# Kernel tuning notes

Hardware: AMD Instinct MI355X
Metric: run time of the kernel (lower is better)

Reference implementation:

```python
import jax, jax.numpy as jnp
import numpy as np

ALPHA = 0.2  # leaky_relu negative slope
NEG_INF = -9e15


def _gat_stage(x, adj_mask, W, a):
    """Multi-head dense GAT layer (concat=True).
    x: [N, Fin], adj_mask: [N, N] bool, W: [H, Fin, O], a: [H, 2*O].
    Returns [N, H*O].
    """
    O = W.shape[-1]
    Wh = jnp.einsum('nf,hfo->hno', x, W)                 # [H, N, O]
    f1 = jnp.einsum('hno,ho->hn', Wh, a[:, :O])          # a_src . Wh_i
    f2 = jnp.einsum('hno,ho->hn', Wh, a[:, O:])          # a_dst . Wh_j
    e = f1[:, :, None] + f2[:, None, :]                  # [H, N, N]
    e = jnp.where(e > 0, e, ALPHA * e)                   # leaky_relu
    e = jnp.where(adj_mask[None], e, NEG_INF)            # mask non-edges
    att = jax.nn.softmax(e, axis=-1)                     # row softmax over neighbors
    h = jnp.einsum('hnm,hmo->hno', att, Wh)              # aggregate
    h = jax.nn.elu(h)                                    # concat=True -> elu
    H, N, _ = h.shape
    return jnp.transpose(h, (1, 0, 2)).reshape(N, H * O)  # head concat


def setup_inputs() -> dict:
    key = jax.random.key(0)
    ks = jax.random.split(key, 12)
    N, F0, NHID, H, NCLASS = 4096, 512, 64, 4, 40
    x = jax.random.normal(ks[0], (N, F0), jnp.float32)
    adj = jax.random.randint(ks[1], (N, N), 0, 2, jnp.int32)
    s = 0.05
    W1 = jax.random.normal(ks[2], (H, F0, NHID), jnp.float32) * s
    a1 = jax.random.normal(ks[3], (H, 2 * NHID), jnp.float32) * s
    W2 = jax.random.normal(ks[4], (4, H * NHID, 32), jnp.float32) * s
    a2 = jax.random.normal(ks[5], (4, 64), jnp.float32) * s
    W3 = jax.random.normal(ks[6], (4, 4 * 32, 16), jnp.float32) * s
    a3 = jax.random.normal(ks[7], (4, 32), jnp.float32) * s
    Wlin = jax.random.normal(ks[8], (4 * 16, NCLASS), jnp.float32) * s
    blin = jnp.zeros((NCLASS,), jnp.float32)
    return {"x": x, "adj": adj, "W1": W1, "a1": a1, "W2": W2, "a2": a2,
            "W3": W3, "a3": a3, "Wlin": Wlin, "blin": blin}


def reference(x, adj, W1, a1, W2, a2, W3, a3, Wlin, blin):
    # eval mode: all F.dropout calls are identity
    m = adj > 0
    h = _gat_stage(x, m, W1, a1)    # [N, 256]
    h = _gat_stage(h, m, W2, a2)    # [N, 128]
    h = _gat_stage(h, m, W3, a3)    # [N, 64]
    logits = h @ Wlin + blin        # [N, nclass]
    return jax.nn.log_softmax(logits, axis=1)
```

## Files before the change

### kernel.cpp

```cpp
#include <hip/hip_runtime.h>
#include <hip/hip_bf16.h>
#include <stdint.h>

typedef __attribute__((ext_vector_type(8))) short short8;
typedef __attribute__((ext_vector_type(4))) float float4v;

#define NHEADS 4
#define NNODES 4096
#define LOG2E 1.4426950408889634f
#define NJS 8
#define PSTR ((size_t)NHEADS * NNODES * 64)
#define LSTR ((size_t)NHEADS * NNODES)

__device__ __forceinline__ unsigned short f2b(float x) {
    union { float f; uint32_t u; } v; v.f = x;
    uint32_t u = v.u;
    uint32_t r = (u + 0x7FFFu + ((u >> 16) & 1u)) >> 16;
    return (unsigned short)r;
}
__device__ __forceinline__ float b2f(unsigned short s) {
    union { uint32_t u; float f; } v; v.u = ((uint32_t)s) << 16;
    return v.f;
}
__device__ __forceinline__ uint32_t cvtpk(float lo, float hi) {
    uint32_t r;
    asm("v_cvt_pk_bf16_f32 %0, %1, %2" : "=v"(r) : "v"(lo), "v"(hi));
    return r;
}

#define AS1 __attribute__((address_space(1)))
#define AS3 __attribute__((address_space(3)))
__device__ __forceinline__ void gl_lds16(const void* g, void* l) {
    __builtin_amdgcn_global_load_lds((const AS1 unsigned int*)g,
                                     (AS3 unsigned int*)l, 16, 0, 0);
}

__global__ __launch_bounds__(256) void k_pre(const int* __restrict__ adj,
                                             unsigned short* __restrict__ mask16,
                                             const float* __restrict__ x,
                                             unsigned short* __restrict__ xbf,
                                             const float* __restrict__ W1,
                                             unsigned short* __restrict__ WT1,
                                             const float* __restrict__ W2,
                                             unsigned short* __restrict__ WT2,
                                             const float* __restrict__ W3,
                                             unsigned short* __restrict__ WT3) {
    int b = blockIdx.x;
    if (b < 4096) {
        const int4* ap = (const int4*)(adj + ((size_t)b << 12)) + threadIdx.x * 4;
        int4 a0 = ap[0], a1 = ap[1], a2 = ap[2], a3 = ap[3];
        int v[16] = {a0.x, a0.y, a0.z, a0.w, a1.x, a1.y, a1.z, a1.w,
                     a2.x, a2.y, a2.z, a2.w, a3.x, a3.y, a3.z, a3.w};
        uint32_t bits = 0;
#pragma unroll
        for (int k = 0; k < 16; ++k) bits |= (uint32_t)(v[k] != 0) << k;
        mask16[(b << 8) + threadIdx.x] = (unsigned short)bits;
        return;
    }
    int i = (b - 4096) * 256 + threadIdx.x;
    if (i < 524288) {
        float4v v = ((const float4v*)x)[i];
        uint2 r;
        r.x = cvtpk(v[0], v[1]);
        r.y = cvtpk(v[2], v[3]);
        ((uint2*)xbf)[i] = r;
    } else if (i < 524288 + 131072) {
        int j = i - 524288;
        int o = j & 63, f = (j >> 6) & 511, h = j >> 15;
        WT1[((size_t)(h * 64 + o)) * 512 + f] = f2b(W1[j]);
    } else if (i < 524288 + 131072 + 32768) {
        int j = i - 655360;
        int o = j & 31, f = (j >> 5) & 255, h = j >> 13;
        WT2[((size_t)(h * 32 + o)) * 256 + f] = f2b(W2[j]);
    } else if (i < 524288 + 131072 + 32768 + 8192) {
        int j = i - 688128;
        int o = j & 15, f = (j >> 4) & 127, h = j >> 11;
        WT3[((size_t)(h * 16 + o)) * 128 + f] = f2b(W3[j]);
    }
}

template <int Fin, int O>
__global__ __launch_bounds__(256) void k_whgemm(const unsigned short* __restrict__ A,
                                                const unsigned short* __restrict__ WT,
                                                const float* __restrict__ avec,
                                                unsigned short* __restrict__ WhT,
                                                float* __restrict__ f1,
                                                float* __restrict__ f2) {
    __shared__ float scc[4][16][64];
    constexpr int HPB = 64 / O;
    const int rt = blockIdx.x & 255, cg = blockIdx.x >> 8;
    const int wv = threadIdx.x >> 6, lane = threadIdx.x & 63;
    const int il = lane & 15, g = lane >> 4;
    constexpr int kpw = Fin >> 2;
    const int k0 = wv * kpw;
    float4v acc[4];
#pragma unroll
    for (int ot = 0; ot < 4; ++ot) acc[ot] = (float4v){0.f, 0.f, 0.f, 0.f};
    const unsigned short* Arow = A + (size_t)(rt * 16 + il) * Fin + k0 + 8 * g;
    const unsigned short* Bcol = WT + (size_t)(cg * 64 + il) * Fin + k0 + 8 * g;
#pragma unroll
    for (int k = 0; k < kpw; k += 32) {
        short8 af = *(const short8*)(Arow + k);
#pragma unroll
        for (int ot = 0; ot < 4; ++ot) {
            short8 bf = *(const short8*)(Bcol + (size_t)ot * 16 * Fin + k);
            acc[ot] = __builtin_amdgcn_mfma_f32_16x16x32_bf16(af, bf, acc[ot], 0, 0, 0);
        }
    }
#pragma unroll
    for (int ot = 0; ot < 4; ++ot)
#pragma unroll
        for (int r = 0; r < 4; ++r) scc[wv][g * 4 + r][ot * 16 + il] = acc[ot][r];
    __syncthreads();
    for (int e = threadIdx.x; e < 1024; e += 256) {
        int row = e >> 6, col = e & 63;
        float v = scc[0][row][col] + scc[1][row][col] + scc[2][row][col] + scc[3][row][col];
        int gc = cg * 64 + col;
        int hh = gc / O, o = gc % O;
        WhT[((size_t)(hh * O + o)) * NNODES + rt * 16 + row] = f2b(v);
    }
    {
        int hl = lane / O, o = lane % O;
        int h = cg * HPB + hl;
        float av1 = avec[h * 2 * O + o];
        float av2 = avec[h * 2 * O + O + o];
#pragma unroll
        for (int r = 0; r < 4; ++r) {
            int row = wv * 4 + r;
            float v = scc[0][row][lane] + scc[1][row][lane] + scc[2][row][lane] + scc[3][row][lane];
            float s1 = v * av1, s2 = v * av2;
#pragma unroll
            for (int d = O / 2; d > 0; d >>= 1) {
                s1 += __shfl_xor(s1, d);
                s2 += __shfl_xor(s2, d);
            }
            if (o == 0) {
                int n = rt * 16 + row;
                f1[h * NNODES + n] = s1 * LOG2E;
                f2[h * NNODES + n] = s2 * LOG2E;
            }
        }
    }
}

template <int O>
__global__ __launch_bounds__(256, 5)
void k_pv(const uint32_t* __restrict__ mask,
          const float* __restrict__ f1L,
          const float* __restrict__ f2L,
          const unsigned short* __restrict__ WhT,
          float* __restrict__ pacc,
          float* __restrict__ lpart) {
    constexpr int TJ  = (O == 16) ? 128 : 64;
    constexpr int NTT = 512 / TJ;
    constexpr int NT  = O / 16;
    constexpr int CH  = O * TJ / 8;
    constexpr int SPT = CH / 256;
    constexpr int CPR = TJ / 8;
    constexpr int NSUB = TJ / 32;
    __shared__ unsigned short bt[3][CH * 8];
    __shared__ float sf2[512];
    const int b = blockIdx.x;
    const int js = b & 7, rt = (b >> 3) & 63, h = b >> 9;
    const int tid = threadIdx.x, wv = tid >> 6, lane = tid & 63;
    const int il = lane & 15, g = lane >> 4;
    const int j0b = js * 512;
    const float* f2h = f2L + h * NNODES;
    const unsigned short* WB0 = WhT + (size_t)h * O * NNODES;
    const int nrow = wv * 16 + il;

    const float f1i = f1L[h * NNODES + rt * 64 + nrow];
    const uint32_t* mrow = mask + (size_t)(rt * 64 + nrow) * 128 + js * 16;
    uint32_t mw[16];
    {
        uint4 a = *(const uint4*)(mrow);
        uint4 c = *(const uint4*)(mrow + 4);
        uint4 d = *(const uint4*)(mrow + 8);
        uint4 e = *(const uint4*)(mrow + 12);
        mw[0] = a.x;  mw[1] = a.y;  mw[2] = a.z;  mw[3] = a.w;
        mw[4] = c.x;  mw[5] = c.y;  mw[6] = c.z;  mw[7] = c.w;
        mw[8] = d.x;  mw[9] = d.y;  mw[10] = d.z; mw[11] = d.w;
        mw[12] = e.x; mw[13] = e.y; mw[14] = e.z; mw[15] = e.w;
    }
    asm volatile("s_waitcnt vmcnt(0)" ::: "memory");
    __builtin_amdgcn_sched_barrier(0);

    auto stage_tile = [&](int t, int buf) {
#pragma unroll
        for (int q = 0; q < SPT; ++q) {
            int s = q * 256 + tid;
            int o = s / CPR, c = s % CPR;
            int cs = c ^ (o & (CPR - 1));
            gl_lds16(WB0 + (size_t)o * NNODES + j0b + t * TJ + 8 * cs,
                     (char*)&bt[buf][0] + s * 16);
        }
    };
    if (tid < 128) gl_lds16(f2h + j0b + tid * 4, (char*)sf2 + tid * 16);
    stage_tile(0, 0);
    stage_tile(1, 1);
    asm volatile("s_waitcnt vmcnt(%0)" :: "i"(SPT) : "memory");
    __builtin_amdgcn_sched_barrier(0);
    __builtin_amdgcn_s_barrier();

    float4v acc[NT];
#pragma unroll
    for (int ot = 0; ot < NT; ++ot) acc[ot] = (float4v){0.f, 0.f, 0.f, 0.f};
    float4v accl = (float4v){0.f, 0.f, 0.f, 0.f};
    short8 bones;
#pragma unroll
    for (int q = 0; q < 8; ++q) bones[q] = (il == 0) ? (short)0x3F80 : (short)0;

    auto compute = [&](int t) {
        const char* btc = (const char*)&bt[t % 3][0];
        const float* fp0 = sf2 + t * TJ + 8 * g;
#pragma unroll
        for (int s = 0; s < NSUB; ++s) {
            short8 B[NT];
#pragma unroll
            for (int ot = 0; ot < NT; ++ot) {
                int o = ot * 16 + il;
                B[ot] = *(const short8*)(btc + o * (CPR * 16) +
                                         16 * (((s << 2) + g) ^ (o & (CPR - 1))));
            }
            const float* fp = fp0 + s * 32;
            float4v fa = *(const float4v*)fp;
            float4v fb = *(const float4v*)(fp + 4);
            uint32_t word = mw[t * NSUB + s];
            uint32_t bits = (word >> (8 * g)) & 0xFFu;
            float p[8];
#pragma unroll
            for (int bb = 0; bb < 8; ++bb) {
                float sv = f1i + ((bb < 4) ? fa[bb] : fb[bb - 4]);
                sv = fmaxf(sv, 0.2f * sv);
                float pv = __builtin_amdgcn_exp2f(sv);
                p[bb] = ((bits >> bb) & 1u) ? pv : 0.f;
            }
            union { short8 s8; uint32_t u[4]; } pu;
            pu.u[0] = cvtpk(p[0], p[1]);
            pu.u[1] = cvtpk(p[2], p[3]);
            pu.u[2] = cvtpk(p[4], p[5]);
            pu.u[3] = cvtpk(p[6], p[7]);
#pragma unroll
            for (int ot = 0; ot < NT; ++ot)
                acc[ot] = __builtin_amdgcn_mfma_f32_16x16x32_bf16(pu.s8, B[ot], acc[ot], 0, 0, 0);
            accl = __builtin_amdgcn_mfma_f32_16x16x32_bf16(pu.s8, bones, accl, 0, 0, 0);
        }
    };

#pragma unroll
    for (int t = 0; t < NTT - 2; ++t) {
        stage_tile(t + 2, (t + 2) % 3);
        compute(t);
        asm volatile("s_waitcnt vmcnt(%0)" :: "i"(SPT) : "memory");
        __builtin_amdgcn_sched_barrier(0);
        __builtin_amdgcn_s_barrier();
    }
    compute(NTT - 2);
    asm volatile("s_waitcnt vmcnt(0)" ::: "memory");
    __builtin_amdgcn_sched_barrier(0);
    __builtin_amdgcn_s_barrier();
    compute(NTT - 1);

    float* pj = pacc + js * PSTR + (size_t)h * NNODES * O;
#pragma unroll
    for (int ot = 0; ot < NT; ++ot)
#pragma unroll
        for (int r = 0; r < 4; ++r)
            pj[(size_t)(rt * 64 + wv * 16 + g * 4 + r) * O + ot * 16 + il] = acc[ot][r];
    if (il == 0) {
        float* lj = lpart + js * LSTR + h * NNODES;
#pragma unroll
        for (int r = 0; r < 4; ++r)
            lj[rt * 64 + wv * 16 + g * 4 + r] = accl[r];
    }
}

template <int O>
__global__ __launch_bounds__(256) void k_fin(const float* __restrict__ pacc,
                                             const float* __restrict__ lpart,
                                             unsigned short* __restrict__ hout) {
    constexpr int HO = NHEADS * O;
    int e = blockIdx.x * 256 + threadIdx.x;
    int o = e % O;
    int n = (e / O) & (NNODES - 1);
    int h = e / (O * NNODES);
    size_t idx = ((size_t)h * NNODES + n) * O + o;
    int li = h * NNODES + n;
    float s = 0.f, l = 0.f;
#pragma unroll
    for (int k = 0; k < NJS; ++k) {
        s += pacc[k * PSTR + idx];
        l += lpart[k * LSTR + li];
    }
    float v = s / l;
    v = (v > 0.f) ? v : (__expf(v) - 1.f);
    hout[(size_t)n * HO + h * O + o] = f2b(v);
}

__global__ __launch_bounds__(256) void k_fin3final(const float* __restrict__ pacc,
                                                   const float* __restrict__ lpart,
                                                   const float* __restrict__ Wlin,
                                                   const float* __restrict__ blin,
                                                   float* __restrict__ out) {
    __shared__ float sh3[4][64];
    const int tid = threadIdx.x;
    const int n0 = blockIdx.x * 4;
    {
        int r = tid >> 6, hh = (tid >> 4) & 3, o = tid & 15;
        int n = n0 + r;
        size_t idx = ((size_t)hh * NNODES + n) * 16 + o;
        int li = hh * NNODES + n;
        float s = 0.f, l = 0.f;
#pragma unroll
        for (int k = 0; k < NJS; ++k) {
            s += pacc[k * PSTR + idx];
            l += lpart[k * LSTR + li];
        }
        float v = s / l;
        v = (v > 0.f) ? v : (__expf(v) - 1.f);
        sh3[r][hh * 16 + o] = v;
    }
    __syncthreads();
    int rr = tid >> 6, lane = tid & 63;
    int n = n0 + rr;
    float logit = 0.f;
    if (lane < 40) {
        logit = blin[lane];
#pragma unroll
        for (int k = 0; k < 64; ++k) logit += sh3[rr][k] * Wlin[k * 40 + lane];
    }
    float mv = (lane < 40) ? logit : -3.0e38f;
    for (int d = 32; d > 0; d >>= 1) mv = fmaxf(mv, __shfl_xor(mv, d));
    float ex = (lane < 40) ? __expf(logit - mv) : 0.f;
    for (int d = 32; d > 0; d >>= 1) ex += __shfl_xor(ex, d);
    if (lane < 40) out[n * 40 + lane] = logit - mv - logf(ex);
}

template <int Fin, int O>
static void run_stage(hipStream_t stream, const uint32_t* mask, const unsigned short* xin,
                      const unsigned short* WT, const float* avec,
                      unsigned short* WhT, float* f1, float* f2,
                      float* pacc, float* lpart) {
    constexpr int CG = (NHEADS * O) / 64;
    k_whgemm<Fin, O><<<256 * CG, 256, 0, stream>>>(xin, WT, avec, WhT, f1, f2);
    k_pv<O><<<4 * 64 * NJS, 256, 0, stream>>>(mask, f1, f2, WhT, pacc, lpart);
}

extern "C" void kernel_launch(void* const* d_in, const int* in_sizes, int n_in,
                              void* d_out, int out_size, void* d_ws, size_t ws_size,
                              hipStream_t stream) {
    const float* x    = (const float*)d_in[0];
    const int*   adj  = (const int*)d_in[1];
    const float* W1   = (const float*)d_in[2];
    const float* a1   = (const float*)d_in[3];
    const float* W2   = (const float*)d_in[4];
    const float* a2   = (const float*)d_in[5];
    const float* W3   = (const float*)d_in[6];
    const float* a3   = (const float*)d_in[7];
    const float* Wlin = (const float*)d_in[8];
    const float* blin = (const float*)d_in[9];
    float* out = (float*)d_out;

    char* ws = (char*)d_ws;
    uint32_t*       mask = (uint32_t*)ws;
    unsigned short* xbf  = (unsigned short*)(ws + (2u << 20));
    unsigned short* WhT  = (unsigned short*)(ws + (6u << 20));
    unsigned short* WT1  = (unsigned short*)(ws + (8u << 20));
    unsigned short* WT2  = (unsigned short*)(ws + (8u << 20) + (256u << 10));
    unsigned short* WT3  = (unsigned short*)(ws + (8u << 20) + (320u << 10));
    float*          f1   = (float*)(ws + (8u << 20) + (384u << 10));
    float*          f2   = (float*)(ws + (8u << 20) + (448u << 10));
    float*          lpart= (float*)(ws + (8u << 20) + (512u << 10));
    float*          pacc = (float*)(ws + (9u << 20));

    k_pre<<<4096 + 2720, 256, 0, stream>>>(adj, (unsigned short*)mask, x, xbf,
                                           W1, WT1, W2, WT2, W3, WT3);

    run_stage<512, 64>(stream, mask, xbf, WT1, a1, WhT, f1, f2, pacc, lpart);
    k_fin<64><<<NHEADS * NNODES * 64 / 256, 256, 0, stream>>>(pacc, lpart, xbf);
    run_stage<256, 32>(stream, mask, xbf, WT2, a2, WhT, f1, f2, pacc, lpart);
    k_fin<32><<<NHEADS * NNODES * 32 / 256, 256, 0, stream>>>(pacc, lpart, xbf);
    run_stage<128, 16>(stream, mask, xbf, WT3, a3, WhT, f1, f2, pacc, lpart);
    k_fin3final<<<NNODES / 4, 256, 0, stream>>>(pacc, lpart, Wlin, blin, out);
}
```

Baseline: 148.1 us.

## Halve j-splits in attention kernel and stage mask bits through LDS

The attention-aggregation kernel now splits the neighbor dimension into 4 chunks of 1024 instead of 8 chunks of 512. Each block covers twice as many tiles, and there are half as many partial accumulators to reduce later. Mask words are loaded cooperatively into a padded shared-memory array instead of 16 registers per thread, which frees registers for the longer loop. Compute sections are wrapped in s_setprio to favor MFMA issue. The cost is fewer blocks, an occupancy hint lowered from 5 to 4, and extra LDS reads for the mask. The combine step may also need to match the new NJS value.

```diff
diff --git a/kernel.cpp b/kernel.cpp
--- a/kernel.cpp
+++ b/kernel.cpp
@@ -8,7 +8,7 @@
 #define NHEADS 4
 #define NNODES 4096
 #define LOG2E 1.4426950408889634f
-#define NJS 8
+#define NJS 4
 #define PSTR ((size_t)NHEADS * NNODES * 64)
 #define LSTR ((size_t)NHEADS * NNODES)
 
@@ -17,10 +17,6 @@
     uint32_t u = v.u;
     uint32_t r = (u + 0x7FFFu + ((u >> 16) & 1u)) >> 16;
     return (unsigned short)r;
-}
-__device__ __forceinline__ float b2f(unsigned short s) {
-    union { uint32_t u; float f; } v; v.u = ((uint32_t)s) << 16;
-    return v.f;
 }
 __device__ __forceinline__ uint32_t cvtpk(float lo, float hi) {
     uint32_t r;
@@ -144,46 +140,44 @@
 }
 
 template <int O>
-__global__ __launch_bounds__(256, 5)
-void k_pv(const uint32_t* __restrict__ mask,
-          const float* __restrict__ f1L,
-          const float* __restrict__ f2L,
-          const unsigned short* __restrict__ WhT,
-          float* __restrict__ pacc,
-          float* __restrict__ lpart) {
-    constexpr int TJ  = (O == 16) ? 128 : 64;
-    constexpr int NTT = 512 / TJ;
-    constexpr int NT  = O / 16;
-    constexpr int CH  = O * TJ / 8;
-    constexpr int SPT = CH / 256;
-    constexpr int CPR = TJ / 8;
+__global__ __launch_bounds__(256, 4) void k_pv(const uint32_t* __restrict__ mask,
+                                               const float* __restrict__ f1L,
+                                               const float* __restrict__ f2L,
+                                               const unsigned short* __restrict__ WhT,
+                                               float* __restrict__ pacc,
+                                               float* __restrict__ lpart) {
+    constexpr int TJ   = (O == 16) ? 128 : 64;
+    constexpr int NTT  = 1024 / TJ;
+    constexpr int NT   = O / 16;
+    constexpr int CH   = O * TJ / 8;
+    constexpr int SPT  = CH / 256;
+    constexpr int CPR  = TJ / 8;
     constexpr int NSUB = TJ / 32;
     __shared__ unsigned short bt[3][CH * 8];
-    __shared__ float sf2[512];
+    __shared__ float sf2[1024];
+    __shared__ uint32_t smask[64][34];
     const int b = blockIdx.x;
-    const int js = b & 7, rt = (b >> 3) & 63, h = b >> 9;
+    const int js = b & 3, rt = (b >> 2) & 63, h = b >> 8;
     const int tid = threadIdx.x, wv = tid >> 6, lane = tid & 63;
     const int il = lane & 15, g = lane >> 4;
-    const int j0b = js * 512;
+    const int j0b = js * 1024;
     const float* f2h = f2L + h * NNODES;
     const unsigned short* WB0 = WhT + (size_t)h * O * NNODES;
     const int nrow = wv * 16 + il;
-
     const float f1i = f1L[h * NNODES + rt * 64 + nrow];
-    const uint32_t* mrow = mask + (size_t)(rt * 64 + nrow) * 128 + js * 16;
-    uint32_t mw[16];
+
     {
-        uint4 a = *(const uint4*)(mrow);
-        uint4 c = *(const uint4*)(mrow + 4);
-        uint4 d = *(const uint4*)(mrow + 8);
-        uint4 e = *(const uint4*)(mrow + 12);
-        mw[0] = a.x;  mw[1] = a.y;  mw[2] = a.z;  mw[3] = a.w;
-        mw[4] = c.x;  mw[5] = c.y;  mw[6] = c.z;  mw[7] = c.w;
-        mw[8] = d.x;  mw[9] = d.y;  mw[10] = d.z; mw[11] = d.w;
-        mw[12] = e.x; mw[13] = e.y; mw[14] = e.z; mw[15] = e.w;
-    }
-    asm volatile("s_waitcnt vmcnt(0)" ::: "memory");
-    __builtin_amdgcn_sched_barrier(0);
+        int r = tid >> 2, c = (tid & 3) * 8;
+        const uint32_t* mg = mask + (size_t)(rt * 64 + r) * 128 + js * 32 + c;
+        uint4 m0 = *(const uint4*)mg;
+        uint4 m1 = *(const uint4*)(mg + 4);
+        asm volatile("s_waitcnt vmcnt(0)" ::: "memory");
+        uint32_t* dstm = &smask[r][c];
+        *(uint2*)(dstm + 0) = make_uint2(m0.x, m0.y);
+        *(uint2*)(dstm + 2) = make_uint2(m0.z, m0.w);
+        *(uint2*)(dstm + 4) = make_uint2(m1.x, m1.y);
+        *(uint2*)(dstm + 6) = make_uint2(m1.z, m1.w);
+    }
 
     auto stage_tile = [&](int t, int buf) {
 #pragma unroll
@@ -195,10 +189,10 @@
                      (char*)&bt[buf][0] + s * 16);
         }
     };
-    if (tid < 128) gl_lds16(f2h + j0b + tid * 4, (char*)sf2 + tid * 16);
+    gl_lds16(f2h + j0b + tid * 4, (char*)sf2 + tid * 16);
     stage_tile(0, 0);
     stage_tile(1, 1);
-    asm volatile("s_waitcnt vmcnt(%0)" :: "i"(SPT) : "memory");
+    asm volatile("s_waitcnt vmcnt(%0) lgkmcnt(0)" :: "i"(SPT) : "memory");
     __builtin_amdgcn_sched_barrier(0);
     __builtin_amdgcn_s_barrier();
 
@@ -213,6 +207,7 @@
     auto compute = [&](int t) {
         const char* btc = (const char*)&bt[t % 3][0];
         const float* fp0 = sf2 + t * TJ + 8 * g;
+        __builtin_amdgcn_s_setprio(1);
 #pragma unroll
         for (int s = 0; s < NSUB; ++s) {
             short8 B[NT];
@@ -225,7 +220,7 @@
             const float* fp = fp0 + s * 32;
             float4v fa = *(const float4v*)fp;
             float4v fb = *(const float4v*)(fp + 4);
-            uint32_t word = mw[t * NSUB + s];
+            uint32_t word = smask[nrow][t * NSUB + s];
             uint32_t bits = (word >> (8 * g)) & 0xFFu;
             float p[8];
 #pragma unroll
@@ -245,6 +240,7 @@
                 acc[ot] = __builtin_amdgcn_mfma_f32_16x16x32_bf16(pu.s8, B[ot], acc[ot], 0, 0, 0);
             accl = __builtin_amdgcn_mfma_f32_16x16x32_bf16(pu.s8, bones, accl, 0, 0, 0);
         }
+        __builtin_amdgcn_s_setprio(0);
     };
 
 #pragma unroll
@@ -343,7 +339,7 @@
                       float* pacc, float* lpart) {
     constexpr int CG = (NHEADS * O) / 64;
     k_whgemm<Fin, O><<<256 * CG, 256, 0, stream>>>(xin, WT, avec, WhT, f1, f2);
-    k_pv<O><<<4 * 64 * NJS, 256, 0, stream>>>(mask, f1, f2, WhT, pacc, lpart);
+    k_pv<O><<<NHEADS * 64 * NJS, 256, 0, stream>>>(mask, f1, f2, WhT, pacc, lpart);
 }
 
 extern "C" void kernel_launch(void* const* d_in, const int* in_sizes, int n_in,
```

Measured after the change: 142.6 us. 1.04x faster.
